# Kernel tuning notes

Hardware: AMD Instinct MI355X
Metric: run time of the kernel (lower is better)

Reference implementation:

```python
import jax, jax.numpy as jnp
import numpy as np

NUM_HEADS = 8
LOCAL_WINDOW = 32


def setup_inputs() -> dict:
    key = jax.random.key(0)
    ks = jax.random.split(key, 5)
    B, T, D = 2, 2048, 512
    s = 1.0 / np.sqrt(D)
    return {
        "x": jax.random.normal(ks[0], (B, T, D), dtype=jnp.float32),
        "Wq": jax.random.normal(ks[1], (D, D), dtype=jnp.float32) * s,
        "bq": jnp.zeros((D,), dtype=jnp.float32),
        "Wk": jax.random.normal(ks[2], (D, D), dtype=jnp.float32) * s,
        "bk": jnp.zeros((D,), dtype=jnp.float32),
        "Wv": jax.random.normal(ks[3], (D, D), dtype=jnp.float32) * s,
        "bv": jnp.zeros((D,), dtype=jnp.float32),
        "Wo": jax.random.normal(ks[4], (D, D), dtype=jnp.float32) * s,
        "bo": jnp.zeros((D,), dtype=jnp.float32),
    }


def reference(x, Wq, bq, Wk, bk, Wv, bv, Wo, bo):
    B, T, D = x.shape
    H = NUM_HEADS
    hd = D // H
    scale = hd ** -0.5
    w = LOCAL_WINDOW

    def proj(W, b):
        # (B,T,D) -> (B,H,T,hd)
        return (x @ W.T + b).reshape(B, T, H, hd).transpose(0, 2, 1, 3)

    q = proj(Wq, bq)
    k = proj(Wk, bk)
    v = proj(Wv, bv)

    scores = jnp.einsum("bhqd,bhkd->bhqk", q, k) * scale  # (B,H,T,T)

    if w < T:
        i = jnp.arange(T)[:, None]
        j = jnp.arange(T)[None, :]
        # row i attends to columns [i - w//2, i + w//2)  (end exclusive)
        allowed = (j >= i - w // 2) & (j < i + w // 2)  # (T,T)
        scores = jnp.where(allowed[None, None], scores, jnp.float32(-jnp.inf))

    attn = jax.nn.softmax(scores, axis=-1)
    out = jnp.einsum("bhqk,bhkd->bhqd", attn, v)  # (B,H,T,hd)
    out = out.transpose(0, 2, 1, 3).reshape(B, T, D)
    return out @ Wo.T + bo
```

## Files before the change

kernel.cpp:

```cpp
#include <hip/hip_runtime.h>

#define B_  2
#define T_  2048
#define D_  512
#define H_  8
#define HD_ 64
#define WHALF_ 16
#define Mtot (B_*T_)
#define QKV_LD 1536

typedef __attribute__((ext_vector_type(8))) short short8;
typedef __attribute__((ext_vector_type(4))) float floatx4;

__device__ __forceinline__ unsigned short f2bf(float f) {
    unsigned u = __float_as_uint(f);
    u = (u + 0x7fffu + ((u >> 16) & 1u)) >> 16;
    return (unsigned short)u;
}

__global__ __launch_bounds__(256) void cast_f32_bf16(
    const float* __restrict__ src, unsigned short* __restrict__ dst, int n4) {
    int i = blockIdx.x * blockDim.x + threadIdx.x;
    if (i < n4) {
        float4 f = ((const float4*)src)[i];
        ushort4 o;
        o.x = f2bf(f.x); o.y = f2bf(f.y); o.z = f2bf(f.z); o.w = f2bf(f.w);
        ((ushort4*)dst)[i] = o;
    }
}

__global__ __launch_bounds__(256) void cast_weights(
    const float* __restrict__ Wq, const float* __restrict__ Wk,
    const float* __restrict__ Wv, const float* __restrict__ Wo,
    const float* __restrict__ bq, const float* __restrict__ bk,
    const float* __restrict__ bv,
    unsigned short* __restrict__ wqkv, unsigned short* __restrict__ wob,
    float* __restrict__ bqkv)
{
    if (blockIdx.x < 1024) {
        int gid = blockIdx.x * 256 + threadIdx.x;
        int m   = gid >> 16;
        int idx = gid & 0xFFFF;
        const float* src = (m == 0) ? Wq : (m == 1) ? Wk : (m == 2) ? Wv : Wo;
        float4 f = ((const float4*)src)[idx];
        ushort4 o;
        o.x = f2bf(f.x); o.y = f2bf(f.y); o.z = f2bf(f.z); o.w = f2bf(f.w);
        if (m < 3) ((ushort4*)wqkv)[(m << 16) + idx] = o;
        else       ((ushort4*)wob)[idx] = o;
    } else {
        for (int i = threadIdx.x; i < 384; i += 256) {
            const float* src = (i < 128) ? bq : (i < 256) ? bk : bv;
            ((float4*)bqkv)[i] = ((const float4*)src)[i & 127];
        }
    }
}

#define GTM 128
#define GTN 64
#define GBK 32
#define ALD 40

template<bool OUT_BF16>
__global__ __launch_bounds__(256) void gemm_bf16_nt(
    const unsigned short* __restrict__ A, const unsigned short* __restrict__ W,
    const float* __restrict__ bias, void* __restrict__ Cv,
    int M, int N, int K)
{
    __shared__ unsigned short As[GTM][ALD];
    __shared__ unsigned short Bs[GTN][ALD];

    const int t  = threadIdx.x;
    const int m0 = blockIdx.x * GTM;
    const int n0 = blockIdx.y * GTN;
    const int w  = t >> 6, l = t & 63;
    const int quad = l >> 4, lo = l & 15;
    const int wm = w & 1, wn = w >> 1;

    const int lrowA0 = t >> 2;
    const int lrowA1 = (t + 256) >> 2;
    const int lko    = (t & 3) * 8;

    floatx4 acc[4][2];
    #pragma unroll
    for (int i = 0; i < 4; ++i)
        #pragma unroll
        for (int j = 0; j < 2; ++j)
            acc[i][j] = (floatx4)0.0f;

    for (int k0 = 0; k0 < K; k0 += GBK) {
        *(short8*)(&As[lrowA0][lko]) =
            *(const short8*)(&A[(size_t)(m0 + lrowA0) * K + k0 + lko]);
        *(short8*)(&As[lrowA1][lko]) =
            *(const short8*)(&A[(size_t)(m0 + lrowA1) * K + k0 + lko]);
        *(short8*)(&Bs[lrowA0][lko]) =
            *(const short8*)(&W[(size_t)(n0 + lrowA0) * K + k0 + lko]);
        __syncthreads();

        short8 b0 = *(const short8*)(&Bs[wn * 32 + lo][quad * 8]);
        short8 b1 = *(const short8*)(&Bs[wn * 32 + 16 + lo][quad * 8]);
        #pragma unroll
        for (int i = 0; i < 4; ++i) {
            short8 a = *(const short8*)(&As[wm * 64 + i * 16 + lo][quad * 8]);
            acc[i][0] = __builtin_amdgcn_mfma_f32_16x16x32_bf16(a, b0, acc[i][0], 0, 0, 0);
            acc[i][1] = __builtin_amdgcn_mfma_f32_16x16x32_bf16(a, b1, acc[i][1], 0, 0, 0);
        }
        __syncthreads();
    }

    #pragma unroll
    for (int i = 0; i < 4; ++i) {
        int rbase = m0 + wm * 64 + i * 16 + quad * 4;
        #pragma unroll
        for (int jn = 0; jn < 2; ++jn) {
            int col = n0 + wn * 32 + jn * 16 + lo;
            float bv = bias[col];
            #pragma unroll
            for (int r = 0; r < 4; ++r) {
                float val = acc[i][jn][r] + bv;
                if constexpr (OUT_BF16)
                    ((unsigned short*)Cv)[(size_t)(rbase + r) * N + col] = f2bf(val);
                else
                    ((float*)Cv)[(size_t)(rbase + r) * N + col] = val;
            }
        }
    }
}

#define KR 96
#define QLD 72
#define VLDP 104

__global__ __launch_bounds__(256) void attn_mfma(
    const unsigned short* __restrict__ qkv, unsigned short* __restrict__ att)
{
    __shared__ unsigned short Qs[64][QLD];
    __shared__ unsigned short Ks[KR][QLD];
    __shared__ unsigned short Vt[64][VLDP];
    __shared__ unsigned short Pws[4][16][VLDP];

    const int q0 = blockIdx.x * 64;
    const int bh = blockIdx.y;
    const int b = bh >> 3, h = bh & 7;
    const int t = threadIdx.x;
    const int wq = t >> 6, l = t & 63;
    const int quad = l >> 4, lo = l & 15;

    const size_t baseQ = (size_t)(b * T_) * QKV_LD + h * HD_;

    for (int c = t; c < 512; c += 256) {
        int row = c >> 3, cg = c & 7;
        *(short8*)(&Qs[row][cg * 8]) =
            *(const short8*)(&qkv[baseQ + (size_t)(q0 + row) * QKV_LD + cg * 8]);
    }
    for (int c = t; c < 768; c += 256) {
        int row = c >> 3, cg = c & 7;
        int g = q0 - WHALF_ + row;
        short8 kv = (short8)(short)0;
        if (g >= 0 && g < T_)
            kv = *(const short8*)(&qkv[baseQ + 512 + (size_t)g * QKV_LD + cg * 8]);
        *(short8*)(&Ks[row][cg * 8]) = kv;
    }
    for (int c = t; c < 768; c += 256) {
        int row = c >> 3, cg = c & 7;
        int g = q0 - WHALF_ + row;
        short8 vv = (short8)(short)0;
        if (g >= 0 && g < T_)
            vv = *(const short8*)(&qkv[baseQ + 1024 + (size_t)g * QKV_LD + cg * 8]);
        #pragma unroll
        for (int j = 0; j < 8; ++j) Vt[cg * 8 + j][row] = vv[j];
    }
    __syncthreads();

    floatx4 S[6];
    #pragma unroll
    for (int kt = 0; kt < 6; ++kt) S[kt] = (floatx4)0.0f;
    short8 aq[2];
    #pragma unroll
    for (int ks = 0; ks < 2; ++ks)
        aq[ks] = *(const short8*)(&Qs[wq * 16 + lo][ks * 32 + quad * 8]);
    #pragma unroll
    for (int kt = 0; kt < 6; ++kt) {
        #pragma unroll
        for (int ks = 0; ks < 2; ++ks) {
            short8 bk8 = *(const short8*)(&Ks[kt * 16 + lo][ks * 32 + quad * 8]);
            S[kt] = __builtin_amdgcn_mfma_f32_16x16x32_bf16(aq[ks], bk8, S[kt], 0, 0, 0);
        }
    }

    float inv_r[4];
    #pragma unroll
    for (int r = 0; r < 4; ++r) {
        int qi = q0 + wq * 16 + quad * 4 + r;
        float mx = -1e30f;
        float sv[6]; bool vd[6];
        #pragma unroll
        for (int kt = 0; kt < 6; ++kt) {
            int j = q0 - WHALF_ + kt * 16 + lo;
            bool ok = (j >= qi - WHALF_) && (j < qi + WHALF_) && (j >= 0) && (j < T_);
            float s = S[kt][r] * 0.125f;
            sv[kt] = s; vd[kt] = ok;
            mx = (ok && s > mx) ? s : mx;
        }
        #pragma unroll
        for (int mm = 1; mm < 16; mm <<= 1) mx = fmaxf(mx, __shfl_xor(mx, mm, 16));
        float den = 0.f;
        #pragma unroll
        for (int kt = 0; kt < 6; ++kt) {
            float e = vd[kt] ? __expf(sv[kt] - mx) : 0.f;
            Pws[wq][quad * 4 + r][kt * 16 + lo] = f2bf(e);
            den += e;
        }
        #pragma unroll
        for (int mm = 1; mm < 16; mm <<= 1) den += __shfl_xor(den, mm, 16);
        inv_r[r] = 1.0f / den;
    }
    __syncthreads();

    floatx4 O[4];
    #pragma unroll
    for (int nt = 0; nt < 4; ++nt) O[nt] = (floatx4)0.0f;
    #pragma unroll
    for (int ks = 0; ks < 3; ++ks) {
        short8 ap = *(const short8*)(&Pws[wq][lo][ks * 32 + quad * 8]);
        #pragma unroll
        for (int nt = 0; nt < 4; ++nt) {
            short8 bv8 = *(const short8*)(&Vt[nt * 16 + lo][ks * 32 + quad * 8]);
            O[nt] = __builtin_amdgcn_mfma_f32_16x16x32_bf16(ap, bv8, O[nt], 0, 0, 0);
        }
    }

    #pragma unroll
    for (int r = 0; r < 4; ++r) {
        int qi = q0 + wq * 16 + quad * 4 + r;
        size_t rowb = (size_t)(b * T_ + qi) * D_ + h * HD_;
        #pragma unroll
        for (int nt = 0; nt < 4; ++nt)
            att[rowb + nt * 16 + lo] = f2bf(O[nt][r] * inv_r[r]);
    }
}

extern "C" void kernel_launch(void* const* d_in, const int* in_sizes, int n_in,
                              void* d_out, int out_size, void* d_ws, size_t ws_size,
                              hipStream_t stream) {
    const float* x  = (const float*)d_in[0];
    const float* Wq = (const float*)d_in[1];
    const float* bq = (const float*)d_in[2];
    const float* Wk = (const float*)d_in[3];
    const float* bk = (const float*)d_in[4];
    const float* Wv = (const float*)d_in[5];
    const float* bv = (const float*)d_in[6];
    const float* Wo = (const float*)d_in[7];
    const float* bo = (const float*)d_in[8];
    float* out = (float*)d_out;

    char* ws = (char*)d_ws;
    unsigned short* xb   = (unsigned short*)(ws);
    unsigned short* wqkv = (unsigned short*)(ws +  4194304);
    unsigned short* wob  = (unsigned short*)(ws +  5767168);
    float*          bqkv = (float*)         (ws +  6291456);
    unsigned short* qkvb = (unsigned short*)(ws +  6297600);
    unsigned short* attb = (unsigned short*)(ws + 18880512);

    cast_f32_bf16<<<2048, 256, 0, stream>>>(x, xb, Mtot * D_ / 4);
    cast_weights<<<1025, 256, 0, stream>>>(Wq, Wk, Wv, Wo, bq, bk, bv,
                                           wqkv, wob, bqkv);

    gemm_bf16_nt<true><<<dim3(Mtot / GTM, QKV_LD / GTN), 256, 0, stream>>>(
        xb, wqkv, bqkv, qkvb, Mtot, QKV_LD, D_);

    attn_mfma<<<dim3(T_ / 64, B_ * H_), 256, 0, stream>>>(qkvb, attb);

    gemm_bf16_nt<false><<<dim3(Mtot / GTM, D_ / GTN), 256, 0, stream>>>(
        attb, wob, bo, out, Mtot, D_, D_);
}
```

Before: 115.1 us.

## Use direct global-to-LDS loads in GEMM, widen QKV tile, merge cast kernels

Replaces the register-staged global-to-shared copies in the bf16 GEMM with global_load_lds 16-byte direct-to-LDS transfers, using an unpadded LDS layout. The QKV projection GEMM gets a 128x128 tile instead of 128x64, and the two cast kernels are merged into one launch. The aim is lower load instruction and register overhead, more reuse per tile, and fewer launches. In exchange, dropping the padding may cause LDS bank conflicts on fragment reads, and the larger tile halves the number of blocks.

```diff
diff --git a/kernel.cpp b/kernel.cpp
--- a/kernel.cpp
+++ b/kernel.cpp
@@ -18,27 +18,30 @@
     return (unsigned short)u;
 }
 
-__global__ __launch_bounds__(256) void cast_f32_bf16(
-    const float* __restrict__ src, unsigned short* __restrict__ dst, int n4) {
-    int i = blockIdx.x * blockDim.x + threadIdx.x;
-    if (i < n4) {
-        float4 f = ((const float4*)src)[i];
-        ushort4 o;
-        o.x = f2bf(f.x); o.y = f2bf(f.y); o.z = f2bf(f.z); o.w = f2bf(f.w);
-        ((ushort4*)dst)[i] = o;
-    }
-}
-
-__global__ __launch_bounds__(256) void cast_weights(
+__device__ __forceinline__ void glds16(const unsigned short* g, unsigned short* l) {
+    __builtin_amdgcn_global_load_lds(
+        (const __attribute__((address_space(1))) void*)g,
+        (__attribute__((address_space(3))) void*)l, 16, 0, 0);
+}
+
+__global__ __launch_bounds__(256) void cast_all(
+    const float* __restrict__ x,
     const float* __restrict__ Wq, const float* __restrict__ Wk,
     const float* __restrict__ Wv, const float* __restrict__ Wo,
     const float* __restrict__ bq, const float* __restrict__ bk,
     const float* __restrict__ bv,
+    unsigned short* __restrict__ xb,
     unsigned short* __restrict__ wqkv, unsigned short* __restrict__ wob,
     float* __restrict__ bqkv)
 {
-    if (blockIdx.x < 1024) {
-        int gid = blockIdx.x * 256 + threadIdx.x;
+    if (blockIdx.x < 2048) {
+        int i = blockIdx.x * 256 + threadIdx.x;
+        float4 f = ((const float4*)x)[i];
+        ushort4 o;
+        o.x = f2bf(f.x); o.y = f2bf(f.y); o.z = f2bf(f.z); o.w = f2bf(f.w);
+        ((ushort4*)xb)[i] = o;
+    } else if (blockIdx.x < 3072) {
+        int gid = (blockIdx.x - 2048) * 256 + threadIdx.x;
         int m   = gid >> 16;
         int idx = gid & 0xFFFF;
         const float* src = (m == 0) ? Wq : (m == 1) ? Wk : (m == 2) ? Wv : Wo;
@@ -55,54 +58,66 @@
     }
 }
 
-#define GTM 128
-#define GTN 64
 #define GBK 32
-#define ALD 40
-
-template<bool OUT_BF16>
+
+template<int TN, bool OUT_BF16>
 __global__ __launch_bounds__(256) void gemm_bf16_nt(
     const unsigned short* __restrict__ A, const unsigned short* __restrict__ W,
     const float* __restrict__ bias, void* __restrict__ Cv,
     int M, int N, int K)
 {
-    __shared__ unsigned short As[GTM][ALD];
-    __shared__ unsigned short Bs[GTN][ALD];
+    constexpr int NJ = TN / 32;
+    __shared__ unsigned short As[128 * GBK];
+    __shared__ unsigned short Bs[TN * GBK];
 
     const int t  = threadIdx.x;
-    const int m0 = blockIdx.x * GTM;
-    const int n0 = blockIdx.y * GTN;
+    const int m0 = blockIdx.x * 128;
+    const int n0 = blockIdx.y * TN;
     const int w  = t >> 6, l = t & 63;
     const int quad = l >> 4, lo = l & 15;
     const int wm = w & 1, wn = w >> 1;
 
-    const int lrowA0 = t >> 2;
-    const int lrowA1 = (t + 256) >> 2;
-    const int lko    = (t & 3) * 8;
-
-    floatx4 acc[4][2];
+    const int lr = l >> 2, lk = (l & 3) * 8;
+    const unsigned short* Ag0 = A + (size_t)(m0 + (2 * w) * 16 + lr) * K + lk;
+    const unsigned short* Ag1 = A + (size_t)(m0 + (2 * w + 1) * 16 + lr) * K + lk;
+    unsigned short* ldsA0 = &As[(2 * w) * 512];
+    unsigned short* ldsA1 = &As[(2 * w + 1) * 512];
+    const unsigned short* Bg0; const unsigned short* Bg1 = nullptr;
+    unsigned short* ldsB0; unsigned short* ldsB1 = nullptr;
+    if constexpr (TN == 128) {
+        Bg0 = W + (size_t)(n0 + (2 * w) * 16 + lr) * K + lk;
+        Bg1 = W + (size_t)(n0 + (2 * w + 1) * 16 + lr) * K + lk;
+        ldsB0 = &Bs[(2 * w) * 512];
+        ldsB1 = &Bs[(2 * w + 1) * 512];
+    } else {
+        Bg0 = W + (size_t)(n0 + w * 16 + lr) * K + lk;
+        ldsB0 = &Bs[w * 512];
+    }
+
+    floatx4 acc[4][NJ];
     #pragma unroll
     for (int i = 0; i < 4; ++i)
         #pragma unroll
-        for (int j = 0; j < 2; ++j)
+        for (int j = 0; j < NJ; ++j)
             acc[i][j] = (floatx4)0.0f;
 
     for (int k0 = 0; k0 < K; k0 += GBK) {
-        *(short8*)(&As[lrowA0][lko]) =
-            *(const short8*)(&A[(size_t)(m0 + lrowA0) * K + k0 + lko]);
-        *(short8*)(&As[lrowA1][lko]) =
-            *(const short8*)(&A[(size_t)(m0 + lrowA1) * K + k0 + lko]);
-        *(short8*)(&Bs[lrowA0][lko]) =
-            *(const short8*)(&W[(size_t)(n0 + lrowA0) * K + k0 + lko]);
+        glds16(Ag0 + k0, ldsA0);
+        glds16(Ag1 + k0, ldsA1);
+        glds16(Bg0 + k0, ldsB0);
+        if constexpr (TN == 128) glds16(Bg1 + k0, ldsB1);
         __syncthreads();
 
-        short8 b0 = *(const short8*)(&Bs[wn * 32 + lo][quad * 8]);
-        short8 b1 = *(const short8*)(&Bs[wn * 32 + 16 + lo][quad * 8]);
+        short8 bf[NJ];
+        #pragma unroll
+        for (int j = 0; j < NJ; ++j)
+            bf[j] = *(const short8*)(&Bs[(wn * (TN / 2) + j * 16 + lo) * GBK + quad * 8]);
         #pragma unroll
         for (int i = 0; i < 4; ++i) {
-            short8 a = *(const short8*)(&As[wm * 64 + i * 16 + lo][quad * 8]);
-            acc[i][0] = __builtin_amdgcn_mfma_f32_16x16x32_bf16(a, b0, acc[i][0], 0, 0, 0);
-            acc[i][1] = __builtin_amdgcn_mfma_f32_16x16x32_bf16(a, b1, acc[i][1], 0, 0, 0);
+            short8 af = *(const short8*)(&As[(wm * 64 + i * 16 + lo) * GBK + quad * 8]);
+            #pragma unroll
+            for (int j = 0; j < NJ; ++j)
+                acc[i][j] = __builtin_amdgcn_mfma_f32_16x16x32_bf16(af, bf[j], acc[i][j], 0, 0, 0);
         }
         __syncthreads();
     }
@@ -111,12 +126,12 @@
     for (int i = 0; i < 4; ++i) {
         int rbase = m0 + wm * 64 + i * 16 + quad * 4;
         #pragma unroll
-        for (int jn = 0; jn < 2; ++jn) {
-            int col = n0 + wn * 32 + jn * 16 + lo;
+        for (int j = 0; j < NJ; ++j) {
+            int col = n0 + wn * (TN / 2) + j * 16 + lo;
             float bv = bias[col];
             #pragma unroll
             for (int r = 0; r < 4; ++r) {
-                float val = acc[i][jn][r] + bv;
+                float val = acc[i][j][r] + bv;
                 if constexpr (OUT_BF16)
                     ((unsigned short*)Cv)[(size_t)(rbase + r) * N + col] = f2bf(val);
                 else
@@ -261,15 +276,14 @@
     unsigned short* qkvb = (unsigned short*)(ws +  6297600);
     unsigned short* attb = (unsigned short*)(ws + 18880512);
 
-    cast_f32_bf16<<<2048, 256, 0, stream>>>(x, xb, Mtot * D_ / 4);
-    cast_weights<<<1025, 256, 0, stream>>>(Wq, Wk, Wv, Wo, bq, bk, bv,
-                                           wqkv, wob, bqkv);
-
-    gemm_bf16_nt<true><<<dim3(Mtot / GTM, QKV_LD / GTN), 256, 0, stream>>>(
+    cast_all<<<3073, 256, 0, stream>>>(x, Wq, Wk, Wv, Wo, bq, bk, bv,
+                                       xb, wqkv, wob, bqkv);
+
+    gemm_bf16_nt<128, true><<<dim3(Mtot / 128, QKV_LD / 128), 256, 0, stream>>>(
         xb, wqkv, bqkv, qkvb, Mtot, QKV_LD, D_);
 
     attn_mfma<<<dim3(T_ / 64, B_ * H_), 256, 0, stream>>>(qkvb, attb);
 
-    gemm_bf16_nt<false><<<dim3(Mtot / GTM, D_ / GTN), 256, 0, stream>>>(
+    gemm_bf16_nt<64, false><<<dim3(Mtot / 128, D_ / 64), 256, 0, stream>>>(
         attb, wob, bo, out, Mtot, D_, D_);
 }
```

Result: no change. 114.1 us (-0.8%).

## Fuse fp32-to-bf16 casts into GEMM tile loads and retile output projection

Applied to the files above, without the earlier changes.

Drops the separate cast kernels for x and the weights. The QKV and output GEMMs now read fp32 directly and convert to bf16 while staging tiles into shared memory, and the QKV GEMM picks Wq/Wk/Wv and the matching bias per column block. This removes two launches and the write and re-read of the bf16 copies. In exchange each tile is converted redundantly across blocks and fp32 global reads double the load bytes. The output GEMM also moves to smaller 64x64 tiles to get more blocks.

```diff
diff --git a/kernel.cpp b/kernel.cpp
--- a/kernel.cpp
+++ b/kernel.cpp
@@ -18,82 +18,54 @@
     return (unsigned short)u;
 }
 
-__global__ __launch_bounds__(256) void cast_f32_bf16(
-    const float* __restrict__ src, unsigned short* __restrict__ dst, int n4) {
-    int i = blockIdx.x * blockDim.x + threadIdx.x;
-    if (i < n4) {
-        float4 f = ((const float4*)src)[i];
-        ushort4 o;
-        o.x = f2bf(f.x); o.y = f2bf(f.y); o.z = f2bf(f.z); o.w = f2bf(f.w);
-        ((ushort4*)dst)[i] = o;
-    }
-}
-
-__global__ __launch_bounds__(256) void cast_weights(
+#define ALD 40
+
+__global__ __launch_bounds__(256) void gemm_qkv(
+    const float* __restrict__ x,
     const float* __restrict__ Wq, const float* __restrict__ Wk,
-    const float* __restrict__ Wv, const float* __restrict__ Wo,
+    const float* __restrict__ Wv,
     const float* __restrict__ bq, const float* __restrict__ bk,
     const float* __restrict__ bv,
-    unsigned short* __restrict__ wqkv, unsigned short* __restrict__ wob,
-    float* __restrict__ bqkv)
+    unsigned short* __restrict__ qkvb)
 {
-    if (blockIdx.x < 1024) {
-        int gid = blockIdx.x * 256 + threadIdx.x;
-        int m   = gid >> 16;
-        int idx = gid & 0xFFFF;
-        const float* src = (m == 0) ? Wq : (m == 1) ? Wk : (m == 2) ? Wv : Wo;
-        float4 f = ((const float4*)src)[idx];
-        ushort4 o;
-        o.x = f2bf(f.x); o.y = f2bf(f.y); o.z = f2bf(f.z); o.w = f2bf(f.w);
-        if (m < 3) ((ushort4*)wqkv)[(m << 16) + idx] = o;
-        else       ((ushort4*)wob)[idx] = o;
-    } else {
-        for (int i = threadIdx.x; i < 384; i += 256) {
-            const float* src = (i < 128) ? bq : (i < 256) ? bk : bv;
-            ((float4*)bqkv)[i] = ((const float4*)src)[i & 127];
-        }
-    }
-}
-
-#define GTM 128
-#define GTN 64
-#define GBK 32
-#define ALD 40
-
-template<bool OUT_BF16>
-__global__ __launch_bounds__(256) void gemm_bf16_nt(
-    const unsigned short* __restrict__ A, const unsigned short* __restrict__ W,
-    const float* __restrict__ bias, void* __restrict__ Cv,
-    int M, int N, int K)
-{
-    __shared__ unsigned short As[GTM][ALD];
-    __shared__ unsigned short Bs[GTN][ALD];
-
-    const int t  = threadIdx.x;
-    const int m0 = blockIdx.x * GTM;
-    const int n0 = blockIdx.y * GTN;
-    const int w  = t >> 6, l = t & 63;
+    __shared__ unsigned short As[128][ALD];
+    __shared__ unsigned short Bs[64][ALD];
+
+    const int t   = threadIdx.x;
+    const int m0  = blockIdx.x * 128;
+    const int n0g = blockIdx.y * 64;
+    const int mat = n0g >> 9;
+    const int n0  = n0g & 511;
+    const float* W    = (mat == 0) ? Wq : (mat == 1) ? Wk : Wv;
+    const float* bias = (mat == 0) ? bq : (mat == 1) ? bk : bv;
+
+    const int w = t >> 6, l = t & 63;
     const int quad = l >> 4, lo = l & 15;
     const int wm = w & 1, wn = w >> 1;
 
-    const int lrowA0 = t >> 2;
-    const int lrowA1 = (t + 256) >> 2;
-    const int lko    = (t & 3) * 8;
-
     floatx4 acc[4][2];
     #pragma unroll
-    for (int i = 0; i < 4; ++i)
-        #pragma unroll
-        for (int j = 0; j < 2; ++j)
-            acc[i][j] = (floatx4)0.0f;
-
-    for (int k0 = 0; k0 < K; k0 += GBK) {
-        *(short8*)(&As[lrowA0][lko]) =
-            *(const short8*)(&A[(size_t)(m0 + lrowA0) * K + k0 + lko]);
-        *(short8*)(&As[lrowA1][lko]) =
-            *(const short8*)(&A[(size_t)(m0 + lrowA1) * K + k0 + lko]);
-        *(short8*)(&Bs[lrowA0][lko]) =
-            *(const short8*)(&W[(size_t)(n0 + lrowA0) * K + k0 + lko]);
+    for (int i = 0; i < 4; ++i) { acc[i][0] = (floatx4)0.0f; acc[i][1] = (floatx4)0.0f; }
+
+    for (int k0 = 0; k0 < 512; k0 += 32) {
+        #pragma unroll
+        for (int p = 0; p < 4; ++p) {
+            int c = t + p * 256;
+            int row = c >> 3, cg = (c & 7) * 4;
+            float4 f = *(const float4*)(&x[(size_t)(m0 + row) * 512 + k0 + cg]);
+            ushort4 o;
+            o.x = f2bf(f.x); o.y = f2bf(f.y); o.z = f2bf(f.z); o.w = f2bf(f.w);
+            *(ushort4*)(&As[row][cg]) = o;
+        }
+        #pragma unroll
+        for (int p = 0; p < 2; ++p) {
+            int c = t + p * 256;
+            int row = c >> 3, cg = (c & 7) * 4;
+            float4 f = *(const float4*)(&W[(size_t)(n0 + row) * 512 + k0 + cg]);
+            ushort4 o;
+            o.x = f2bf(f.x); o.y = f2bf(f.y); o.z = f2bf(f.z); o.w = f2bf(f.w);
+            *(ushort4*)(&Bs[row][cg]) = o;
+        }
         __syncthreads();
 
         short8 b0 = *(const short8*)(&Bs[wn * 32 + lo][quad * 8]);
@@ -111,17 +83,67 @@
     for (int i = 0; i < 4; ++i) {
         int rbase = m0 + wm * 64 + i * 16 + quad * 4;
         #pragma unroll
-        for (int jn = 0; jn < 2; ++jn) {
-            int col = n0 + wn * 32 + jn * 16 + lo;
-            float bv = bias[col];
+        for (int j = 0; j < 2; ++j) {
+            int colm = n0 + wn * 32 + j * 16 + lo;
+            int colg = n0g + wn * 32 + j * 16 + lo;
+            float bv = bias[colm];
             #pragma unroll
-            for (int r = 0; r < 4; ++r) {
-                float val = acc[i][jn][r] + bv;
-                if constexpr (OUT_BF16)
-                    ((unsigned short*)Cv)[(size_t)(rbase + r) * N + col] = f2bf(val);
-                else
-                    ((float*)Cv)[(size_t)(rbase + r) * N + col] = val;
-            }
+            for (int r = 0; r < 4; ++r)
+                qkvb[(size_t)(rbase + r) * QKV_LD + colg] = f2bf(acc[i][j][r] + bv);
+        }
+    }
+}
+
+__global__ __launch_bounds__(256) void gemm_out(
+    const unsigned short* __restrict__ attb, const float* __restrict__ Wo,
+    const float* __restrict__ bo, float* __restrict__ out)
+{
+    __shared__ unsigned short As[64][ALD];
+    __shared__ unsigned short Bs[64][ALD];
+
+    const int t  = threadIdx.x;
+    const int m0 = blockIdx.x * 64;
+    const int n0 = blockIdx.y * 64;
+    const int w = t >> 6, l = t & 63;
+    const int quad = l >> 4, lo = l & 15;
+
+    floatx4 acc[4];
+    #pragma unroll
+    for (int j = 0; j < 4; ++j) acc[j] = (floatx4)0.0f;
+
+    const int arow = t >> 2, ako = (t & 3) * 8;
+
+    for (int k0 = 0; k0 < 512; k0 += 32) {
+        *(short8*)(&As[arow][ako]) =
+            *(const short8*)(&attb[(size_t)(m0 + arow) * 512 + k0 + ako]);
+        #pragma unroll
+        for (int p = 0; p < 2; ++p) {
+            int c = t + p * 256;
+            int row = c >> 3, cg = (c & 7) * 4;
+            float4 f = *(const float4*)(&Wo[(size_t)(n0 + row) * 512 + k0 + cg]);
+            ushort4 o;
+            o.x = f2bf(f.x); o.y = f2bf(f.y); o.z = f2bf(f.z); o.w = f2bf(f.w);
+            *(ushort4*)(&Bs[row][cg]) = o;
+        }
+        __syncthreads();
+
+        short8 a = *(const short8*)(&As[w * 16 + lo][quad * 8]);
+        #pragma unroll
+        for (int j = 0; j < 4; ++j) {
+            short8 b = *(const short8*)(&Bs[j * 16 + lo][quad * 8]);
+            acc[j] = __builtin_amdgcn_mfma_f32_16x16x32_bf16(a, b, acc[j], 0, 0, 0);
+        }
+        __syncthreads();
+    }
+
+    #pragma unroll
+    for (int j = 0; j < 4; ++j) {
+        int col = n0 + j * 16 + lo;
+        float bv = bo[col];
+        #pragma unroll
+        for (int r = 0; r < 4; ++r) {
+            int row = m0 + w * 16 + quad * 4 + r;
+            out[(size_t)row * 512 + col] = acc[j][r] + bv;
         }
     }
 }
@@ -254,22 +276,13 @@
     float* out = (float*)d_out;
 
     char* ws = (char*)d_ws;
-    unsigned short* xb   = (unsigned short*)(ws);
-    unsigned short* wqkv = (unsigned short*)(ws +  4194304);
-    unsigned short* wob  = (unsigned short*)(ws +  5767168);
-    float*          bqkv = (float*)         (ws +  6291456);
-    unsigned short* qkvb = (unsigned short*)(ws +  6297600);
-    unsigned short* attb = (unsigned short*)(ws + 18880512);
-
-    cast_f32_bf16<<<2048, 256, 0, stream>>>(x, xb, Mtot * D_ / 4);
-    cast_weights<<<1025, 256, 0, stream>>>(Wq, Wk, Wv, Wo, bq, bk, bv,
-                                           wqkv, wob, bqkv);
-
-    gemm_bf16_nt<true><<<dim3(Mtot / GTM, QKV_LD / GTN), 256, 0, stream>>>(
-        xb, wqkv, bqkv, qkvb, Mtot, QKV_LD, D_);
+    unsigned short* qkvb = (unsigned short*)(ws);
+    unsigned short* attb = (unsigned short*)(ws + 12582912);
+
+    gemm_qkv<<<dim3(Mtot / 128, QKV_LD / 64), 256, 0, stream>>>(
+        x, Wq, Wk, Wv, bq, bk, bv, qkvb);
 
     attn_mfma<<<dim3(T_ / 64, B_ * H_), 256, 0, stream>>>(qkvb, attb);
 
-    gemm_bf16_nt<false><<<dim3(Mtot / GTM, D_ / GTN), 256, 0, stream>>>(
-        attb, wob, bo, out, Mtot, D_, D_);
-}
+    gemm_out<<<dim3(Mtot / 64, D_ / 64), 256, 0, stream>>>(attb, Wo, bo, out);
+}
```

Result: slower. 141.5 us (+23.0%).
